# Performance work log

Measured on AMD Instinct MI355X. Metric: run time of the kernel, lower is better.

Reference implementation:

```python
import jax, jax.numpy as jnp
import numpy as np

B, S, V, E, H, C = 1024, 128, 32000, 512, 1024, 512


def setup_inputs() -> dict:
    key = jax.random.key(0)
    ks = jax.random.split(key, 12)
    x_in = jax.random.randint(ks[0], (B, S), 0, V, dtype=jnp.int32)
    x_lengths = jax.random.randint(ks[1], (B,), 1, S + 1, dtype=jnp.int32)  # in [1, S]

    def nrm(k, shape, scale):
        return jax.random.normal(k, shape, dtype=jnp.float32) * scale

    emb_table = nrm(ks[2], (V, E), 0.02).at[0].set(0.0)  # padding_idx=0 row zeroed
    s_ih = 1.0 / np.sqrt(H)
    W_ih = nrm(ks[3], (H, E), s_ih)
    W_hh = nrm(ks[4], (H, H), s_ih)
    b_ih = nrm(ks[5], (H,), s_ih)
    b_hh = nrm(ks[6], (H,), s_ih)
    W1 = nrm(ks[7], (H, H), 1.0 / np.sqrt(H))
    b1 = nrm(ks[8], (H,), 0.01)
    W2 = nrm(ks[9], (C, H), 1.0 / np.sqrt(H))
    b2 = nrm(ks[10], (C,), 0.01)
    return {
        "x_in": x_in, "x_lengths": x_lengths, "emb_table": emb_table,
        "W_ih": W_ih, "W_hh": W_hh, "b_ih": b_ih, "b_hh": b_hh,
        "W1": W1, "b1": b1, "W2": W2, "b2": b2,
    }


def reference(x_in, x_lengths, emb_table, W_ih, W_hh, b_ih, b_hh, W1, b1, W2, b2):
    # Embedding lookup: (B, S, E)
    x_emb = emb_table[x_in]
    x_seq = jnp.swapaxes(x_emb, 0, 1)  # (S, B, E) for the time scan
    batch = x_in.shape[0]
    h0 = jnp.zeros((batch, W_hh.shape[0]), dtype=x_emb.dtype)

    def step(h, x_t):
        # Elman RNNCell: h' = tanh(x W_ih^T + b_ih + h W_hh^T + b_hh)
        h = jnp.tanh(x_t @ W_ih.T + b_ih + h @ W_hh.T + b_hh)
        return h, h

    _, hs = jax.lax.scan(step, h0, x_seq)  # (S, B, H)
    # column_gather: final hidden at position len-1 per sequence
    y = hs[x_lengths - 1, jnp.arange(batch)]  # (B, H)
    # MLP head (dropout is identity in eval mode)
    y = jax.nn.relu(y @ W1.T + b1)
    return y @ W2.T + b2  # (B, C) logits (apply_softmax=False)
```

## Files before the change

### kernel.cpp

```cpp
#include <hip/hip_runtime.h>

typedef unsigned short u16;
constexpr int Ss = 128, Hn = 1024, En = 512, Cn = 512, Vn = 32000;
constexpr size_t PL = 1024u * 1024u;

using short8 = __attribute__((ext_vector_type(8))) short;
using f32x4  = __attribute__((ext_vector_type(4))) float;

__device__ __align__(1024) u16 g_hh[2][PL];
__device__ __align__(1024) u16 g_hl[2][PL];
__device__ __align__(1024) u16 g_yh[PL], g_yl[PL];
__device__ __align__(1024) u16 g_zh[PL], g_zl[PL];
__device__ __align__(1024) float g_proj[(size_t)Vn * Hn];
__device__ int g_perm[1024];
__device__ int g_lsort[1024];
__device__ __align__(1024) u16 t_eh[(size_t)Vn * En], t_el[(size_t)Vn * En];
__device__ __align__(1024) u16 t_xh[(size_t)Hn * En], t_xl[(size_t)Hn * En];
__device__ __align__(1024) u16 t_hh[(size_t)Hn * Hn], t_hl[(size_t)Hn * Hn];
__device__ __align__(1024) u16 t_1h[(size_t)Hn * Hn], t_1l[(size_t)Hn * Hn];
__device__ __align__(1024) u16 t_2h[(size_t)Cn * Hn], t_2l[(size_t)Cn * Hn];

__device__ __forceinline__ void gl16(const void* g, void* l) {
  __builtin_amdgcn_global_load_lds((const __attribute__((address_space(1))) void*)g,
                                   (__attribute__((address_space(3))) void*)l, 16, 0, 0);
}
__device__ __forceinline__ unsigned f2bf(float f) {
  unsigned u = __float_as_uint(f);
  return (u + 0x7fffu + ((u >> 16) & 1u)) >> 16;
}
__device__ __forceinline__ float bf2f(unsigned u) { return __uint_as_float(u << 16); }

__global__ void sort_k(const int* __restrict__ x_len) {
  const int i = threadIdx.x;
  const int li = x_len[i];
  int rank = 0;
  for (int j = 0; j < 1024; ++j) {
    const int lj = x_len[j];
    rank += (lj > li) || (lj == li && j < i);
  }
  g_perm[rank] = i;
  g_lsort[rank] = li;
}

__global__ void cvt_all(const float* __restrict__ emb, const float* __restrict__ Wih,
                        const float* __restrict__ Whh, const float* __restrict__ W1,
                        const float* __restrict__ W2) {
  constexpr size_t N0 = (size_t)Vn * En;
  constexpr size_t N1 = N0 + (size_t)Hn * En;
  constexpr size_t N2 = N1 + (size_t)Hn * Hn;
  constexpr size_t N3 = N2 + (size_t)Hn * Hn;
  constexpr size_t N4 = N3 + (size_t)Cn * Hn;
  const size_t stride = (size_t)gridDim.x * blockDim.x;
  for (size_t i = (size_t)blockIdx.x * blockDim.x + threadIdx.x; i < N4; i += stride) {
    const float* src; u16 *hi, *lo; size_t o;
    if (i < N0)      { src = emb; hi = t_eh; lo = t_el; o = i; }
    else if (i < N1) { src = Wih; hi = t_xh; lo = t_xl; o = i - N0; }
    else if (i < N2) { src = Whh; hi = t_hh; lo = t_hl; o = i - N1; }
    else if (i < N3) { src = W1;  hi = t_1h; lo = t_1l; o = i - N2; }
    else             { src = W2;  hi = t_2h; lo = t_2l; o = i - N3; }
    const float v = src[o];
    const unsigned h = f2bf(v);
    hi[o] = (u16)h;
    lo[o] = (u16)f2bf(v - bf2f(h));
  }
}

#define GEMM_PROLOG_NOBID()                                                    \
  const int tid = threadIdx.x;                                                 \
  const int w = tid >> 6, l = tid & 63;                                        \
  const int wr = w & 3, wc = w >> 2;                                           \
  const int lrow = l & 15, lk = l >> 4;                                        \
  const int sr = tid >> 3, p = tid & 7;                                        \
  const int sby = ((p ^ (sr & 7)) << 4);                                       \
  const int arow = (wr << 4) + lrow;                                           \
  int aoff[2], bboff[2][2];                                                    \
  _Pragma("unroll") for (int s = 0; s < 2; ++s)                                \
      aoff[s] = arow * 128 + ((s * 64 + lk * 16) ^ ((arow & 7) << 4));         \
  _Pragma("unroll") for (int n = 0; n < 2; ++n) {                              \
    const int jl = (wc << 5) + (n << 4) + lrow;                                \
    _Pragma("unroll") for (int s = 0; s < 2; ++s)                              \
        bboff[n][s] = jl * 128 + ((s * 64 + lk * 16) ^ ((jl & 7) << 4));       \
  }
#define GEMM_PROLOG() const int bid = blockIdx.x; GEMM_PROLOG_NOBID()

#define GEMM_MFMA(ca, cb)                                                      \
  _Pragma("unroll") for (int s = 0; s < 2; ++s) {                              \
    short8 a = *(const short8*)((ca) + aoff[s]);                               \
    _Pragma("unroll") for (int n = 0; n < 2; ++n) {                            \
      short8 b = *(const short8*)((cb) + bboff[n][s]);                         \
      acc[n] = __builtin_amdgcn_mfma_f32_16x16x32_bf16(a, b, acc[n], 0, 0, 0); \
    }                                                                          \
  }

__global__ void __launch_bounds__(512) proj_k(const float* __restrict__ bih,
                                              const float* __restrict__ bhh) {
  extern __shared__ char ring[];
  const int tid = threadIdx.x, bid = blockIdx.x;
  const int w = tid >> 6, l = tid & 63;
  const int wr = w & 3, wc = w >> 2;
  const int lrow = l & 15, lk = l >> 4;
  const int sr = tid >> 3, p = tid & 7;
  const int sby = ((p ^ (sr & 7)) << 4);
  const int sby2 = ((p ^ ((sr + 64) & 7)) << 4);
  const int v0 = (bid % 500) << 6;
  const int j0 = (bid / 500) << 7;

  const int arow = (wr << 4) + lrow;
  int aoff[2], bboff[4][2];
#pragma unroll
  for (int s = 0; s < 2; ++s)
    aoff[s] = arow * 128 + ((s * 64 + lk * 16) ^ ((arow & 7) << 4));
#pragma unroll
  for (int n = 0; n < 4; ++n) {
    const int jl = (wc << 6) + (n << 4) + lrow;
#pragma unroll
    for (int s = 0; s < 2; ++s)
      bboff[n][s] = jl * 128 + ((s * 64 + lk * 16) ^ ((jl & 7) << 4));
  }

  f32x4 acc[4];
#pragma unroll
  for (int n = 0; n < 4; ++n) {
    const float bs = bih[j0 + (wc << 6) + (n << 4) + lrow] +
                     bhh[j0 + (wc << 6) + (n << 4) + lrow];
#pragma unroll
    for (int ri = 0; ri < 4; ++ri) acc[n][ri] = bs;
  }

  auto stage = [&](int c) {
    char* sl = ring + (c & 1) * 49152;
    const int kb = c * 128;
    gl16((const char*)t_eh + (size_t)(v0 + sr) * 1024 + kb + sby, sl + w * 1024);
    gl16((const char*)t_el + (size_t)(v0 + sr) * 1024 + kb + sby, sl + 8192 + w * 1024);
    gl16((const char*)t_xh + (size_t)(j0 + sr) * 1024 + kb + sby, sl + 16384 + w * 1024);
    gl16((const char*)t_xh + (size_t)(j0 + 64 + sr) * 1024 + kb + sby2,
         sl + 24576 + w * 1024);
    gl16((const char*)t_xl + (size_t)(j0 + sr) * 1024 + kb + sby, sl + 32768 + w * 1024);
    gl16((const char*)t_xl + (size_t)(j0 + 64 + sr) * 1024 + kb + sby2,
         sl + 40960 + w * 1024);
  };
  stage(0); stage(1);
  for (int c = 0; c < 8; ++c) {
    if (c < 7) asm volatile("s_waitcnt vmcnt(6)" ::: "memory");
    else       asm volatile("s_waitcnt vmcnt(0)" ::: "memory");
    __builtin_amdgcn_s_barrier();
    __builtin_amdgcn_sched_barrier(0);
    const char* sl = ring + (c & 1) * 49152;
#pragma unroll
    for (int s = 0; s < 2; ++s) {
      short8 aH = *(const short8*)(sl + aoff[s]);
      short8 aL = *(const short8*)(sl + 8192 + aoff[s]);
#pragma unroll
      for (int n = 0; n < 4; ++n) {
        short8 bH = *(const short8*)(sl + 16384 + bboff[n][s]);
        short8 bL = *(const short8*)(sl + 32768 + bboff[n][s]);
        acc[n] = __builtin_amdgcn_mfma_f32_16x16x32_bf16(aH, bH, acc[n], 0, 0, 0);
        acc[n] = __builtin_amdgcn_mfma_f32_16x16x32_bf16(aL, bH, acc[n], 0, 0, 0);
        acc[n] = __builtin_amdgcn_mfma_f32_16x16x32_bf16(aH, bL, acc[n], 0, 0, 0);
      }
    }
    __builtin_amdgcn_s_barrier();
    if (c + 2 < 8) stage(c + 2);
  }
#pragma unroll
  for (int n = 0; n < 4; ++n) {
    const int j = j0 + (wc << 6) + (n << 4) + lrow;
#pragma unroll
    for (int ri = 0; ri < 4; ++ri)
      g_proj[(size_t)(v0 + (wr << 4) + lk * 4 + ri) * 1024 + j] = acc[n][ri];
  }
}

__global__ void __launch_bounds__(512) step_k(const int* __restrict__ x_in, int t) {
  extern __shared__ char ring[];
  __shared__ int toks[64];
  GEMM_PROLOG()
  const int b0 = (bid & 15) << 6, j0 = (bid >> 4) << 6;

  if (g_lsort[b0] <= t) return;

  const u16* hinh = g_hh[t & 1];
  const u16* hinl = g_hl[t & 1];
  u16* houth = g_hh[(t + 1) & 1];
  u16* houtl = g_hl[(t + 1) & 1];

  if (tid < 64) toks[tid] = x_in[g_perm[b0 + tid] * Ss + t];
  __syncthreads();

  float pj[2][4];
#pragma unroll
  for (int n = 0; n < 2; ++n) {
    const int j = j0 + (wc << 5) + (n << 4) + lrow;
#pragma unroll
    for (int ri = 0; ri < 4; ++ri)
      pj[n][ri] = g_proj[(size_t)toks[(wr << 4) + lk * 4 + ri] * 1024 + j];
  }
  asm volatile("" ::: "memory");

  f32x4 acc[2];
  acc[0] = (f32x4){0.f, 0.f, 0.f, 0.f}; acc[1] = acc[0];

  if (t > 0) {
    auto stage = [&](int c) {
      char* sl = ring + (c & 3) * 32768;
      const int kb = c * 128;
      gl16((const char*)hinh + (size_t)(b0 + sr) * 2048 + kb + sby, sl + w * 1024);
      gl16((const char*)hinl + (size_t)(b0 + sr) * 2048 + kb + sby, sl + 8192 + w * 1024);
      gl16((const char*)t_hh + (size_t)(j0 + sr) * 2048 + kb + sby, sl + 16384 + w * 1024);
      gl16((const char*)t_hl + (size_t)(j0 + sr) * 2048 + kb + sby, sl + 24576 + w * 1024);
    };
    stage(0); stage(1); stage(2);
    for (int c = 0; c < 16; ++c) {
      const int left = 15 - c;
      if (left >= 2)      asm volatile("s_waitcnt vmcnt(8)" ::: "memory");
      else if (left == 1) asm volatile("s_waitcnt vmcnt(4)" ::: "memory");
      else                asm volatile("s_waitcnt vmcnt(0)" ::: "memory");
      __builtin_amdgcn_s_barrier();
      __builtin_amdgcn_sched_barrier(0);
      if (c + 3 < 16) stage(c + 3);
      const char* sl = ring + (c & 3) * 32768;
#pragma unroll
      for (int s = 0; s < 2; ++s) {
        short8 aH = *(const short8*)(sl + aoff[s]);
        short8 aL = *(const short8*)(sl + 8192 + aoff[s]);
#pragma unroll
        for (int n = 0; n < 2; ++n) {
          short8 bH = *(const short8*)(sl + 16384 + bboff[n][s]);
          short8 bL = *(const short8*)(sl + 24576 + bboff[n][s]);
          acc[n] = __builtin_amdgcn_mfma_f32_16x16x32_bf16(aH, bH, acc[n], 0, 0, 0);
          acc[n] = __builtin_amdgcn_mfma_f32_16x16x32_bf16(aL, bH, acc[n], 0, 0, 0);
          acc[n] = __builtin_amdgcn_mfma_f32_16x16x32_bf16(aH, bL, acc[n], 0, 0, 0);
        }
      }
    }
  }

#pragma unroll
  for (int n = 0; n < 2; ++n) {
    const int j = j0 + (wc << 5) + (n << 4) + lrow;
#pragma unroll
    for (int ri = 0; ri < 4; ++ri) {
      const int brow = b0 + (wr << 4) + lk * 4 + ri;
      const float v = tanhf(acc[n][ri] + pj[n][ri]);
      const unsigned hi = f2bf(v);
      const unsigned lo = f2bf(v - bf2f(hi));
      const size_t off = (size_t)brow * 1024 + j;
      houth[off] = (u16)hi;
      houtl[off] = (u16)lo;
      if (g_lsort[brow] == t + 1) { g_yh[off] = (u16)hi; g_yl[off] = (u16)lo; }
    }
  }
}

__global__ void __launch_bounds__(512) mlp_k(const float* __restrict__ bias,
                                             float* __restrict__ out, int mode) {
  __shared__ char sA[16384];
  __shared__ char sB[16384];
  GEMM_PROLOG()
  const int b0 = (bid & 15) << 6, j0 = (bid >> 4) << 6;
  const u16* ah = mode ? g_zh : g_yh;
  const u16* al = mode ? g_zl : g_yl;
  const u16* bh = mode ? t_2h : t_1h;
  const u16* bl = mode ? t_2l : t_1l;

  f32x4 acc[2];
#pragma unroll
  for (int n = 0; n < 2; ++n) {
    const float bs = bias[j0 + (wc << 5) + (n << 4) + lrow];
#pragma unroll
    for (int ri = 0; ri < 4; ++ri) acc[n][ri] = bs;
  }

  auto stage = [&](int c) {
    char* da = sA + (c & 1) * 8192;
    char* db = sB + (c & 1) * 8192;
    const u16* ap = (c >= 16 && c < 32) ? al : ah;
    const u16* bp = (c < 32) ? bh : bl;
    const int kb = (c & 15) * 128;
    gl16((const char*)ap + (size_t)(b0 + sr) * 2048 + kb + sby, da + w * 1024);
    gl16((const char*)bp + (size_t)(j0 + sr) * 2048 + kb + sby, db + w * 1024);
  };
  stage(0);
  __syncthreads();
  for (int c = 0; c < 48; ++c) {
    const char* ca = sA + (c & 1) * 8192;
    const char* cb = sB + (c & 1) * 8192;
    if (c < 47) stage(c + 1);
    GEMM_MFMA(ca, cb)
    __syncthreads();
  }

#pragma unroll
  for (int n = 0; n < 2; ++n) {
    const int j = j0 + (wc << 5) + (n << 4) + lrow;
#pragma unroll
    for (int ri = 0; ri < 4; ++ri) {
      const int brow = b0 + (wr << 4) + lk * 4 + ri;
      if (mode == 0) {
        const float v = fmaxf(acc[n][ri], 0.f);
        const unsigned hi = f2bf(v);
        const unsigned lo = f2bf(v - bf2f(hi));
        const size_t off = (size_t)brow * 1024 + j;
        g_zh[off] = (u16)hi;
        g_zl[off] = (u16)lo;
      } else {
        out[(size_t)g_perm[brow] * 512 + j] = acc[n][ri];
      }
    }
  }
}

extern "C" void kernel_launch(void* const* d_in, const int* in_sizes, int n_in,
                              void* d_out, int out_size, void* d_ws, size_t ws_size,
                              hipStream_t stream) {
  const int*   x_in  = (const int*)d_in[0];
  const int*   x_len = (const int*)d_in[1];
  const float* emb = (const float*)d_in[2];
  const float* Wih = (const float*)d_in[3];
  const float* Whh = (const float*)d_in[4];
  const float* bih = (const float*)d_in[5];
  const float* bhh = (const float*)d_in[6];
  const float* W1  = (const float*)d_in[7];
  const float* b1  = (const float*)d_in[8];
  const float* W2  = (const float*)d_in[9];
  const float* b2  = (const float*)d_in[10];
  float* out = (float*)d_out;

  (void)hipFuncSetAttribute((const void*)step_k,
                            hipFuncAttributeMaxDynamicSharedMemorySize, 131072);
  (void)hipFuncSetAttribute((const void*)proj_k,
                            hipFuncAttributeMaxDynamicSharedMemorySize, 98304);

  sort_k<<<dim3(1), dim3(1024), 0, stream>>>(x_len);
  cvt_all<<<dim3(4096), dim3(256), 0, stream>>>(emb, Wih, Whh, W1, W2);

  proj_k<<<dim3(4000), dim3(512), 98304, stream>>>(bih, bhh);

  for (int t = 0; t < Ss; ++t)
    step_k<<<dim3(256), dim3(512), 131072, stream>>>(x_in, t);

  mlp_k<<<dim3(256), dim3(512), 0, stream>>>(b1, nullptr, 0);
  mlp_k<<<dim3(128), dim3(512), 0, stream>>>(b2, out, 1);
}
```

Measured before the change: 1.736 ms.

## Halve step_k output tile to 64x32 and launch 512 blocks per timestep

The recurrent step kernel now gives each block a 64-row by 32-column output tile instead of 64x64, so each timestep launches 512 blocks instead of 256 and uses more of the CUs. The LDS ring drops from four 32KB stages to three 24KB stages with prefetch depth 2. The weight tile is loaded by split warps (hi and lo halves). Each block now does half the MFMA work but still stages the full 64-row h tile, so h is read from global memory twice as often, and the shallower pipeline may expose more load latency.

```diff
diff --git a/kernel.cpp b/kernel.cpp
--- a/kernel.cpp
+++ b/kernel.cpp
@@ -174,10 +174,31 @@
 __global__ void __launch_bounds__(512) step_k(const int* __restrict__ x_in, int t) {
   extern __shared__ char ring[];
   __shared__ int toks[64];
-  GEMM_PROLOG()
-  const int b0 = (bid & 15) << 6, j0 = (bid >> 4) << 6;
+  const int tid = threadIdx.x, bid = blockIdx.x;
+  const int w = tid >> 6, l = tid & 63;
+  const int wr = w & 3, wc = w >> 2;
+  const int lrow = l & 15, lk = l >> 4;
+  const int b0 = (bid & 15) << 6, j0 = (bid >> 4) << 5;
 
   if (g_lsort[b0] <= t) return;
+
+  const int arow = (wr << 4) + lrow;
+  int aoff[2], boff[2];
+  const int jl = (wc << 4) + lrow;
+#pragma unroll
+  for (int s = 0; s < 2; ++s) {
+    aoff[s] = arow * 128 + ((s * 64 + lk * 16) ^ ((arow & 7) << 4));
+    boff[s] = jl * 128 + ((s * 64 + lk * 16) ^ ((jl & 7) << 4));
+  }
+
+  const int arow8 = (w << 3) + (l >> 3);
+  const int acolb = ((l & 7) ^ (arow8 & 7)) << 4;
+  const size_t aSrc = (size_t)(b0 + arow8) * 2048 + acolb;
+  const int wrow8 = ((w & 3) << 3) + (l >> 3);
+  const int wcolb = ((l & 7) ^ (wrow8 & 7)) << 4;
+  const size_t wSrc = (size_t)(j0 + wrow8) * 2048 + wcolb;
+  const u16* wsrc = (w < 4) ? t_hh : t_hl;
+  const int wDst = ((w < 4) ? 16384 : 20480) + (w & 3) * 1024;
 
   const u16* hinh = g_hh[t & 1];
   const u16* hinl = g_hl[t & 1];
@@ -187,68 +208,54 @@
   if (tid < 64) toks[tid] = x_in[g_perm[b0 + tid] * Ss + t];
   __syncthreads();
 
-  float pj[2][4];
-#pragma unroll
-  for (int n = 0; n < 2; ++n) {
-    const int j = j0 + (wc << 5) + (n << 4) + lrow;
-#pragma unroll
-    for (int ri = 0; ri < 4; ++ri)
-      pj[n][ri] = g_proj[(size_t)toks[(wr << 4) + lk * 4 + ri] * 1024 + j];
-  }
+  float pj[4];
+#pragma unroll
+  for (int ri = 0; ri < 4; ++ri)
+    pj[ri] = g_proj[(size_t)toks[(wr << 4) + lk * 4 + ri] * 1024 + j0 + jl];
   asm volatile("" ::: "memory");
 
-  f32x4 acc[2];
-  acc[0] = (f32x4){0.f, 0.f, 0.f, 0.f}; acc[1] = acc[0];
+  f32x4 acc = (f32x4){0.f, 0.f, 0.f, 0.f};
 
   if (t > 0) {
     auto stage = [&](int c) {
-      char* sl = ring + (c & 3) * 32768;
-      const int kb = c * 128;
-      gl16((const char*)hinh + (size_t)(b0 + sr) * 2048 + kb + sby, sl + w * 1024);
-      gl16((const char*)hinl + (size_t)(b0 + sr) * 2048 + kb + sby, sl + 8192 + w * 1024);
-      gl16((const char*)t_hh + (size_t)(j0 + sr) * 2048 + kb + sby, sl + 16384 + w * 1024);
-      gl16((const char*)t_hl + (size_t)(j0 + sr) * 2048 + kb + sby, sl + 24576 + w * 1024);
+      char* sl = ring + (c % 3) * 24576;
+      const size_t kb = (size_t)c * 128;
+      gl16((const char*)hinh + aSrc + kb, sl + w * 1024);
+      gl16((const char*)hinl + aSrc + kb, sl + 8192 + w * 1024);
+      gl16((const char*)wsrc + wSrc + kb, sl + wDst);
     };
-    stage(0); stage(1); stage(2);
+    stage(0); stage(1);
     for (int c = 0; c < 16; ++c) {
-      const int left = 15 - c;
-      if (left >= 2)      asm volatile("s_waitcnt vmcnt(8)" ::: "memory");
-      else if (left == 1) asm volatile("s_waitcnt vmcnt(4)" ::: "memory");
-      else                asm volatile("s_waitcnt vmcnt(0)" ::: "memory");
+      if (c < 15) asm volatile("s_waitcnt vmcnt(3)" ::: "memory");
+      else        asm volatile("s_waitcnt vmcnt(0)" ::: "memory");
       __builtin_amdgcn_s_barrier();
       __builtin_amdgcn_sched_barrier(0);
-      if (c + 3 < 16) stage(c + 3);
-      const char* sl = ring + (c & 3) * 32768;
+      if (c + 2 < 16) stage(c + 2);
+      const char* sl = ring + (c % 3) * 24576;
 #pragma unroll
       for (int s = 0; s < 2; ++s) {
         short8 aH = *(const short8*)(sl + aoff[s]);
         short8 aL = *(const short8*)(sl + 8192 + aoff[s]);
-#pragma unroll
-        for (int n = 0; n < 2; ++n) {
-          short8 bH = *(const short8*)(sl + 16384 + bboff[n][s]);
-          short8 bL = *(const short8*)(sl + 24576 + bboff[n][s]);
-          acc[n] = __builtin_amdgcn_mfma_f32_16x16x32_bf16(aH, bH, acc[n], 0, 0, 0);
-          acc[n] = __builtin_amdgcn_mfma_f32_16x16x32_bf16(aL, bH, acc[n], 0, 0, 0);
-          acc[n] = __builtin_amdgcn_mfma_f32_16x16x32_bf16(aH, bL, acc[n], 0, 0, 0);
-        }
+        short8 bH = *(const short8*)(sl + 16384 + boff[s]);
+        short8 bL = *(const short8*)(sl + 20480 + boff[s]);
+        acc = __builtin_amdgcn_mfma_f32_16x16x32_bf16(aH, bH, acc, 0, 0, 0);
+        acc = __builtin_amdgcn_mfma_f32_16x16x32_bf16(aL, bH, acc, 0, 0, 0);
+        acc = __builtin_amdgcn_mfma_f32_16x16x32_bf16(aH, bL, acc, 0, 0, 0);
       }
     }
   }
 
-#pragma unroll
-  for (int n = 0; n < 2; ++n) {
-    const int j = j0 + (wc << 5) + (n << 4) + lrow;
-#pragma unroll
-    for (int ri = 0; ri < 4; ++ri) {
-      const int brow = b0 + (wr << 4) + lk * 4 + ri;
-      const float v = tanhf(acc[n][ri] + pj[n][ri]);
-      const unsigned hi = f2bf(v);
-      const unsigned lo = f2bf(v - bf2f(hi));
-      const size_t off = (size_t)brow * 1024 + j;
-      houth[off] = (u16)hi;
-      houtl[off] = (u16)lo;
-      if (g_lsort[brow] == t + 1) { g_yh[off] = (u16)hi; g_yl[off] = (u16)lo; }
-    }
+  const int j = j0 + jl;
+#pragma unroll
+  for (int ri = 0; ri < 4; ++ri) {
+    const int brow = b0 + (wr << 4) + lk * 4 + ri;
+    const float v = tanhf(acc[ri] + pj[ri]);
+    const unsigned hi = f2bf(v);
+    const unsigned lo = f2bf(v - bf2f(hi));
+    const size_t off = (size_t)brow * 1024 + j;
+    houth[off] = (u16)hi;
+    houtl[off] = (u16)lo;
+    if (g_lsort[brow] == t + 1) { g_yh[off] = (u16)hi; g_yl[off] = (u16)lo; }
   }
 }
 
@@ -327,7 +334,7 @@
   float* out = (float*)d_out;
 
   (void)hipFuncSetAttribute((const void*)step_k,
-                            hipFuncAttributeMaxDynamicSharedMemorySize, 131072);
+                            hipFuncAttributeMaxDynamicSharedMemorySize, 73728);
   (void)hipFuncSetAttribute((const void*)proj_k,
                             hipFuncAttributeMaxDynamicSharedMemorySize, 98304);
 
@@ -337,7 +344,7 @@
   proj_k<<<dim3(4000), dim3(512), 98304, stream>>>(bih, bhh);
 
   for (int t = 0; t < Ss; ++t)
-    step_k<<<dim3(256), dim3(512), 131072, stream>>>(x_in, t);
+    step_k<<<dim3(512), dim3(512), 73728, stream>>>(x_in, t);
 
   mlp_k<<<dim3(256), dim3(512), 0, stream>>>(b1, nullptr, 0);
   mlp_k<<<dim3(128), dim3(512), 0, stream>>>(b2, out, 1);
```

Result: slower. 1.852 ms (+6.7%).
